# Kernel tuning notes

Measured on AMD Instinct MI355X. Metric: run time of the kernel, lower is better.

Reference implementation:

```python
import jax, jax.numpy as jnp
import numpy as np

B, D, F = 4096, 2048, 16384


def setup_inputs() -> dict:
    key = jax.random.key(0)
    ks = jax.random.split(key, 5)
    s_enc = 1.0 / np.sqrt(D)
    s_dec = 1.0 / np.sqrt(F)
    return {
        "x": jax.random.normal(ks[0], (B, D), dtype=jnp.float32),
        "W_enc": jax.random.normal(ks[1], (F, D), dtype=jnp.float32) * s_enc,
        "b_enc": jnp.zeros((F,), dtype=jnp.float32),
        "W_kest1": jax.random.normal(ks[2], (F, D), dtype=jnp.float32) * s_enc,
        "b_kest1": jnp.zeros((F,), dtype=jnp.float32),
        "W_kest2": jax.random.normal(ks[3], (1, F), dtype=jnp.float32) * s_dec,
        "b_kest2": jnp.zeros((1,), dtype=jnp.float32),
        "W_dec": jax.random.normal(ks[4], (D, F), dtype=jnp.float32) * s_dec,
        "b_dec": jnp.zeros((D,), dtype=jnp.float32),
        "k": 64,
    }


def topk_per_row(acts, k_est):
    # rank of each element when sorted descending (ties resolved stably;
    # after ReLU ties are zeros, so output is identical either way)
    order = jnp.argsort(-acts, axis=1)          # [B, F] descending order
    rank = jnp.argsort(order, axis=1)           # rank[i,j] = position of acts[i,j]
    mask = rank < k_est[:, None]                # per-row dynamic (float) k
    return acts * mask


def reference(x, W_enc, b_enc, W_kest1, b_kest1, W_kest2, b_kest2, W_dec, b_dec, k):
    xc = x - b_dec                                              # [B, D]
    acts = jax.nn.relu(xc @ W_enc.T + b_enc)                    # [B, F]
    h = jax.nn.relu(xc @ W_kest1.T + b_kest1)                   # [B, F]
    k_est = jax.nn.sigmoid(h @ W_kest2.T + b_kest2)[:, 0] * (2.0 * k)  # [B]
    enc = topk_per_row(acts, k_est)                             # [B, F] sparse codes
    x_hat = enc @ W_dec.T + b_dec                               # [B, D]
    return x_hat
```

## Files before the change

kernel.cpp:

```cpp
#include <hip/hip_runtime.h>
#include <hip/hip_bf16.h>
#include <cstdint>
#include <cstddef>

#define BATCH 4096
#define DIM   2048
#define FEAT  16384
#define MAXF  2048

typedef __attribute__((ext_vector_type(8))) short s8v;
typedef __attribute__((ext_vector_type(8))) _Float16 h8v;
typedef __attribute__((ext_vector_type(4))) float f4v;

__device__ __forceinline__ void split2(float v, unsigned short &h, unsigned short &l){
  _Float16 hf = (_Float16)v;
  _Float16 lf = (_Float16)((v - (float)hf) * 2048.0f);
  h = __builtin_bit_cast(unsigned short, hf);
  l = __builtin_bit_cast(unsigned short, lf);
}

__device__ __forceinline__ void gload16(const void* g, void* l){
  __builtin_amdgcn_global_load_lds(
      (const __attribute__((address_space(1))) void*)g,
      (__attribute__((address_space(3))) void*)l, 16, 0, 0);
}

__global__ __launch_bounds__(256)
void splitX(const float* __restrict__ x, const float* __restrict__ bdec,
            unsigned short* __restrict__ p0, unsigned short* __restrict__ p1)
{
  const size_t i = ((size_t)blockIdx.x * 256 + threadIdx.x) * 4;
  const int col = (int)(i & (DIM - 1));
  const float4 v = *(const float4*)(x + i);
  const float4 b = *(const float4*)(bdec + col);
  float e0 = v.x - b.x, e1 = v.y - b.y, e2 = v.z - b.z, e3 = v.w - b.w;
  ushort4 H, L;
  split2(e0, H.x, L.x); split2(e1, H.y, L.y);
  split2(e2, H.z, L.z); split2(e3, H.w, L.w);
  *(ushort4*)(p0 + i) = H; *(ushort4*)(p1 + i) = L;
}

__global__ __launch_bounds__(256)
void splitW(const float* __restrict__ w,
            unsigned short* __restrict__ p0, unsigned short* __restrict__ p1)
{
  const size_t i = ((size_t)blockIdx.x * 256 + threadIdx.x) * 4;
  const float4 v = *(const float4*)(w + i);
  ushort4 H, L;
  split2(v.x, H.x, L.x); split2(v.y, H.y, L.y);
  split2(v.z, H.z, L.z); split2(v.w, H.w, L.w);
  *(ushort4*)(p0 + i) = H; *(ushort4*)(p1 + i) = L;
}

__global__ __launch_bounds__(256)
void splitW1(const float* __restrict__ w, unsigned short* __restrict__ p0)
{
  const size_t i = ((size_t)blockIdx.x * 256 + threadIdx.x) * 4;
  const float4 v = *(const float4*)(w + i);
  ushort4 H;
  H.x = __builtin_bit_cast(unsigned short, (_Float16)v.x);
  H.y = __builtin_bit_cast(unsigned short, (_Float16)v.y);
  H.z = __builtin_bit_cast(unsigned short, (_Float16)v.z);
  H.w = __builtin_bit_cast(unsigned short, (_Float16)v.w);
  *(ushort4*)(p0 + i) = H;
}

__global__ __launch_bounds__(512, 3)
void gemmd(const unsigned short* __restrict__ Ah_, const unsigned short* __restrict__ B1h_,
           const unsigned short* __restrict__ B2h_,
           const float* __restrict__ benc, const float* __restrict__ bk1,
           const float* __restrict__ w2,
           float* __restrict__ acts, float* __restrict__ zpart)
{
  __shared__ unsigned short sAB[2][3][128][32];
  const int tid  = threadIdx.x;
  const int lane = tid & 63, wv = tid >> 6;

  const int bid = blockIdx.x;
  const int xcd = bid & 7;
  const int idx = bid >> 3;
  const int sq  = idx >> 6;
  const int s   = idx & 63;
  const int bx  = (xcd << 4) | ((sq & 1) << 3) | (s & 7);
  const int by  = ((sq >> 1) << 3) | (s >> 3);
  const int row0 = by << 7, col0 = bx << 7;

  const int role = wv >> 2;
  const int wloc = wv & 3;
  const int wr = (wloc & 1) << 6, wc = (wloc >> 1) << 6;

  f4v acc[4][4];
  #pragma unroll
  for (int i = 0; i < 4; ++i)
    #pragma unroll
    for (int j = 0; j < 4; ++j)
      acc[i][j] = (f4v){0.f, 0.f, 0.f, 0.f};

  const unsigned short* gsrc[3];
  unsigned ldsoff[3];
  #pragma unroll
  for (int j = 0; j < 3; ++j){
    const int q = wv * 3 + j;
    const int mat = q >> 3;
    const int chunk = q & 7;
    const int r  = (chunk << 4) + (lane >> 2);
    const int gl = (lane & 3) ^ ((r >> 1) & 3);
    const int rowg = ((mat == 0) ? row0 : col0) + r;
    const unsigned short* P = (mat == 0) ? Ah_ : ((mat == 1) ? B1h_ : B2h_);
    gsrc[j]  = P + (size_t)rowg * DIM + (gl << 3);
    ldsoff[j] = (unsigned)(mat * 8192 + chunk * 1024);
  }

  const int fr16 = lane & 15;
  const int kg   = lane >> 4;
  const int bmat = 1 + role;
  int ra[4], rb[4];
  #pragma unroll
  for (int f = 0; f < 4; ++f){ ra[f] = wr + (f << 4) + fr16; rb[f] = wc + (f << 4) + fr16; }

  #define LDFRAGD(bf, mat, r) \
    (*(const h8v*)((const char*)sAB + (bf) * 24576 + (mat) * 8192 + (r) * 64 + (((kg ^ (((r) >> 1) & 3)) << 4))))
  #define STAGED(bf, ko)                                                      \
    {                                                                         \
      _Pragma("unroll")                                                       \
      for (int j = 0; j < 3; ++j)                                             \
        gload16(gsrc[j] + (ko), (char*)sAB + (bf) * 24576 + ldsoff[j]);       \
    }

  int cur = 0;
  STAGED(0, 0);
  __syncthreads();

  for (int kt = 0; kt < DIM / 32; ++kt){
    if (kt < DIM / 32 - 1) STAGED(cur ^ 1, (kt + 1) << 5);

    h8v Ahf[4], Bhf[4];
    #pragma unroll
    for (int f = 0; f < 4; ++f) Ahf[f] = LDFRAGD(cur, 0, ra[f]);
    #pragma unroll
    for (int f = 0; f < 4; ++f) Bhf[f] = LDFRAGD(cur, bmat, rb[f]);
    #pragma unroll
    for (int fi = 0; fi < 4; ++fi)
      #pragma unroll
      for (int fj = 0; fj < 4; ++fj)
        acc[fi][fj] = __builtin_amdgcn_mfma_f32_16x16x32_f16(Bhf[fj], Ahf[fi], acc[fi][fj], 0, 0, 0);

    __syncthreads();
    cur ^= 1;
  }
  #undef LDFRAGD
  #undef STAGED

  const int mloc = lane & 15;
  const int nq   = (lane >> 4) << 2;
  if (role == 0){
    #pragma unroll
    for (int fi = 0; fi < 4; ++fi){
      const int grow = row0 + wr + (fi << 4) + mloc;
      #pragma unroll
      for (int fj = 0; fj < 4; ++fj){
        const int gcol = col0 + wc + (fj << 4) + nq;
        const float4 be = *(const float4*)(benc + gcol);
        f4v v;
        v[0] = fmaxf(acc[fi][fj][0] + be.x, 0.f);
        v[1] = fmaxf(acc[fi][fj][1] + be.y, 0.f);
        v[2] = fmaxf(acc[fi][fj][2] + be.z, 0.f);
        v[3] = fmaxf(acc[fi][fj][3] + be.w, 0.f);
        __builtin_nontemporal_store(v, (f4v*)(acts + (size_t)grow * FEAT + gcol));
      }
    }
  } else {
    #pragma unroll
    for (int fi = 0; fi < 4; ++fi){
      float ssum = 0.f;
      #pragma unroll
      for (int fj = 0; fj < 4; ++fj){
        const int gcol = col0 + wc + (fj << 4) + nq;
        const float4 be = *(const float4*)(bk1 + gcol);
        const float4 wk = *(const float4*)(w2 + gcol);
        float h0 = fmaxf(acc[fi][fj][0] + be.x, 0.f);
        float h1 = fmaxf(acc[fi][fj][1] + be.y, 0.f);
        float h2 = fmaxf(acc[fi][fj][2] + be.z, 0.f);
        float h3 = fmaxf(acc[fi][fj][3] + be.w, 0.f);
        ssum = fmaf(h0, wk.x, ssum);
        ssum = fmaf(h1, wk.y, ssum);
        ssum = fmaf(h2, wk.z, ssum);
        ssum = fmaf(h3, wk.w, ssum);
      }
      ssum += __shfl_xor(ssum, 16);
      ssum += __shfl_xor(ssum, 32);
      if (lane < 16){
        const int grow = row0 + wr + (fi << 4) + lane;
        zpart[(size_t)grow * 256 + (bx << 1) + (wc >> 6)] = ssum;
      }
    }
  }
}

__global__ __launch_bounds__(512, 4)
void gemmx(const unsigned short* __restrict__ Ah_, const unsigned short* __restrict__ Al_,
           const unsigned short* __restrict__ Bh_, const unsigned short* __restrict__ Bl_,
           const float* __restrict__ bias, const float* __restrict__ w2,
           const int* __restrict__ rowList, const int* __restrict__ nflagp,
           float* __restrict__ zexact)
{
  const int panel = blockIdx.x >> 7;
  const int bx    = blockIdx.x & 127;
  const int row0p = panel << 7;
  if (row0p >= *nflagp) return;
  const int col0 = bx << 7;

  __shared__ unsigned short sAB[2][2][128][64];
  const int tid  = threadIdx.x;
  const int lane = tid & 63, wv = tid >> 6;
  const int wr = (wv & 3) << 5, wc = (wv >> 2) << 6;

  f4v acc[2][4], acc2[2][4];
  #pragma unroll
  for (int i = 0; i < 2; ++i)
    #pragma unroll
    for (int j = 0; j < 4; ++j){
      acc[i][j]  = (f4v){0.f, 0.f, 0.f, 0.f};
      acc2[i][j] = (f4v){0.f, 0.f, 0.f, 0.f};
    }

  const unsigned short* gsrc[4];
  unsigned ldsoff[4];
  #pragma unroll
  for (int j = 0; j < 4; ++j){
    const int q = (wv << 2) + j;
    const int mat = q >> 4;
    const int chunk = q & 15;
    const int r  = (chunk << 3) + (lane >> 3);
    const int gl = (lane & 7) ^ (r & 7);
    const int co = (gl & 3) << 3;
    const unsigned short* hi = (mat == 0) ? Ah_ : Bh_;
    const unsigned short* lo = (mat == 0) ? Al_ : Bl_;
    const int rowg = (mat == 0) ? rowList[row0p + r] : (col0 + r);
    gsrc[j]  = ((gl < 4) ? hi : lo) + (size_t)rowg * DIM + co;
    ldsoff[j] = (unsigned)(mat * 16384 + chunk * 1024);
  }

  const int fr16 = lane & 15;
  const int kg   = lane >> 4;
  int ra[2], rb[4];
  #pragma unroll
  for (int f = 0; f < 2; ++f) ra[f] = wr + (f << 4) + fr16;
  #pragma unroll
  for (int f = 0; f < 4; ++f) rb[f] = wc + (f << 4) + fr16;

  #define LDFRAG(bf, mat, r, hb) \
    (*(const h8v*)((const char*)sAB + (bf) * 32768 + (mat) * 16384 + (r) * 128 + (((((hb) + kg) ^ ((r) & 7)) << 4))))
  #define STAGE(bf, ko)                                                       \
    {                                                                         \
      _Pragma("unroll")                                                       \
      for (int j = 0; j < 4; ++j)                                             \
        gload16(gsrc[j] + (ko), (char*)sAB + (bf) * 32768 + ldsoff[j]);       \
    }

  int cur = 0;
  STAGE(0, 0);
  __syncthreads();

  for (int kt = 0; kt < DIM / 32; ++kt){
    if (kt < DIM / 32 - 1) STAGE(cur ^ 1, (kt + 1) << 5);

    h8v Ahf[2], Bhf[4], Xl[4];
    #pragma unroll
    for (int f = 0; f < 2; ++f) Ahf[f] = LDFRAG(cur, 0, ra[f], 0);
    #pragma unroll
    for (int f = 0; f < 4; ++f) Bhf[f] = LDFRAG(cur, 1, rb[f], 0);
    #pragma unroll
    for (int fi = 0; fi < 2; ++fi)
      #pragma unroll
      for (int fj = 0; fj < 4; ++fj)
        acc[fi][fj] = __builtin_amdgcn_mfma_f32_16x16x32_f16(Bhf[fj], Ahf[fi], acc[fi][fj], 0, 0, 0);
    #pragma unroll
    for (int f = 0; f < 2; ++f) Xl[f] = LDFRAG(cur, 0, ra[f], 4);
    #pragma unroll
    for (int fi = 0; fi < 2; ++fi)
      #pragma unroll
      for (int fj = 0; fj < 4; ++fj)
        acc2[fi][fj] = __builtin_amdgcn_mfma_f32_16x16x32_f16(Bhf[fj], Xl[fi], acc2[fi][fj], 0, 0, 0);
    #pragma unroll
    for (int f = 0; f < 4; ++f) Xl[f] = LDFRAG(cur, 1, rb[f], 4);
    #pragma unroll
    for (int fi = 0; fi < 2; ++fi)
      #pragma unroll
      for (int fj = 0; fj < 4; ++fj)
        acc2[fi][fj] = __builtin_amdgcn_mfma_f32_16x16x32_f16(Xl[fj], Ahf[fi], acc2[fi][fj], 0, 0, 0);

    __syncthreads();
    cur ^= 1;
  }
  #undef LDFRAG
  #undef STAGE

  const float LSC = 1.0f / 2048.0f;
  const int nq = (lane >> 4) << 2;
  #pragma unroll
  for (int fi = 0; fi < 2; ++fi){
    float ssum = 0.f;
    #pragma unroll
    for (int fj = 0; fj < 4; ++fj){
      const int gcol = col0 + wc + (fj << 4) + nq;
      const float4 be = *(const float4*)(bias + gcol);
      const float4 wk = *(const float4*)(w2 + gcol);
      float h0 = fmaxf(acc[fi][fj][0] + LSC * acc2[fi][fj][0] + be.x, 0.f);
      float h1 = fmaxf(acc[fi][fj][1] + LSC * acc2[fi][fj][1] + be.y, 0.f);
      float h2 = fmaxf(acc[fi][fj][2] + LSC * acc2[fi][fj][2] + be.z, 0.f);
      float h3 = fmaxf(acc[fi][fj][3] + LSC * acc2[fi][fj][3] + be.w, 0.f);
      ssum = fmaf(h0, wk.x, ssum);
      ssum = fmaf(h1, wk.y, ssum);
      ssum = fmaf(h2, wk.z, ssum);
      ssum = fmaf(h3, wk.w, ssum);
    }
    ssum += __shfl_xor(ssum, 16);
    ssum += __shfl_xor(ssum, 32);
    if (lane < 16){
      const int pos = row0p + wr + (fi << 4) + lane;
      zexact[(size_t)pos * 256 + (bx << 1) + (wc >> 6)] = ssum;
    }
  }
}

__global__ __launch_bounds__(256)
void zinit(int* __restrict__ rowList, int* __restrict__ nflag)
{
  const int i = blockIdx.x * 256 + threadIdx.x;
  if (i < MAXF) rowList[i] = 0;
  if (i == 0) *nflag = 0;
}

__global__ __launch_bounds__(256)
void zreduce_flag(const float* __restrict__ zpart, const float* __restrict__ bk2,
                  const int* __restrict__ kp, int* __restrict__ mrow,
                  int* __restrict__ rowList, int* __restrict__ nflag)
{
  const int row  = blockIdx.x * 4 + (threadIdx.x >> 6);
  const int lane = threadIdx.x & 63;
  const float* zp = zpart + (size_t)row * 256;
  float s = zp[lane] + zp[lane + 64] + zp[lane + 128] + zp[lane + 192];
  s += __shfl_xor(s, 1);
  s += __shfl_xor(s, 2);
  s += __shfl_xor(s, 4);
  s += __shfl_xor(s, 8);
  s += __shfl_xor(s, 16);
  s += __shfl_xor(s, 32);
  if (lane == 0){
    float z = s + bk2[0];
    float kest = 2.f * (float)(*kp) * (1.f / (1.f + expf(-z)));
    int m = (int)ceilf(kest);
    m = min(max(m, 0), 128);
    mrow[row] = m;
    const float frac = kest - floorf(kest);
    const float dmin = fminf(frac, 1.f - frac);
    if (dmin < 0.1f){
      int p = atomicAdd(nflag, 1);
      if (p < MAXF) rowList[p] = row;
    }
  }
}

__global__ __launch_bounds__(256)
void zreduce2(const float* __restrict__ zexact, const int* __restrict__ rowList,
              const int* __restrict__ nflagp, const float* __restrict__ bk2,
              const int* __restrict__ kp, int* __restrict__ mrow)
{
  const int pos  = blockIdx.x * 4 + (threadIdx.x >> 6);
  const int lane = threadIdx.x & 63;
  const int nf = min(*nflagp, MAXF);
  if (pos >= nf) return;
  const float* zp = zexact + (size_t)pos * 256;
  float s = zp[lane] + zp[lane + 64] + zp[lane + 128] + zp[lane + 192];
  s += __shfl_xor(s, 1);
  s += __shfl_xor(s, 2);
  s += __shfl_xor(s, 4);
  s += __shfl_xor(s, 8);
  s += __shfl_xor(s, 16);
  s += __shfl_xor(s, 32);
  if (lane == 0){
    float z = s + bk2[0];
    float kest = 2.f * (float)(*kp) * (1.f / (1.f + expf(-z)));
    int m = (int)ceilf(kest);
    m = min(max(m, 0), 128);
    mrow[rowList[pos]] = m;
  }
}

__device__ __forceinline__ void radix_find(int* hist, int nbins, int need, int tid,
                                           int* out3, int* blksum)
{
  const int per  = nbins >> 8;
  const int base = tid * per;
  int bs = 0;
  for (int j = 0; j < per; ++j) bs += hist[base + j];
  blksum[tid] = bs;
  __syncthreads();
  if (tid == 0){
    int a2 = 0;
    for (int t = 255; t >= 0; --t){ int v = blksum[t]; blksum[t] = a2; a2 += v; }
  }
  __syncthreads();
  int ch = blksum[tid];
  for (int j = per - 1; j >= 0; --j){
    const int b = base + j;
    const int c = hist[b];
    if (ch < need && need <= ch + c){ out3[0] = b; out3[1] = need - ch; out3[2] = ch; }
    ch += c;
  }
  __syncthreads();
}

__global__ __launch_bounds__(256)
void select_band(const float* __restrict__ acts, const float* __restrict__ x,
                 const float* __restrict__ bdec, const float* __restrict__ Wenc,
                 const int* __restrict__ mrow, int* __restrict__ selIdx,
                 float* __restrict__ selVal, int* __restrict__ scount)
{
  __shared__ int hist[2048];
  __shared__ int blksum[256];
  __shared__ int out3[4];
  __shared__ unsigned listU[2048];
  __shared__ int listI[2048];
  __shared__ int lcnt, dcnt, acnt;
  __shared__ unsigned ambU[64];
  __shared__ int ambI[64];
  __shared__ double ambE[64];
  __shared__ double wred[4];

  const int row = blockIdx.x, tid = threadIdx.x;
  const int m = mrow[row];
  const float* rp = acts + (size_t)row * FEAT;
  const int base = row << 7;

  for (int i = tid; i < 2048; i += 256) hist[i] = 0;
  __syncthreads();
  for (int it = 0; it < 16; ++it){
    const int i4 = (it << 8) + tid;
    const uint4 u4 = *(const uint4*)(rp + ((size_t)i4 << 2));
    if (u4.x) atomicAdd(&hist[u4.x >> 21], 1);
    if (u4.y) atomicAdd(&hist[u4.y >> 21], 1);
    if (u4.z) atomicAdd(&hist[u4.z >> 21], 1);
    if (u4.w) atomicAdd(&hist[u4.w >> 21], 1);
  }
  __syncthreads();
  radix_find(hist, 2048, m, tid, out3, blksum);
  const int bin1 = out3[0];
  const int rem1 = out3[1];
  const int bin1m1 = (bin1 > 1) ? bin1 - 1 : 1;

  if (tid == 0){ lcnt = 0; dcnt = 0; acnt = 0; }
  __syncthreads();
  for (int it = 0; it < 16; ++it){
    const int i4 = (it << 8) + tid;
    const uint4 u4 = *(const uint4*)(rp + ((size_t)i4 << 2));
    const int ib = i4 << 2;
    if (u4.x && (int)(u4.x >> 21) >= bin1m1){ int p = atomicAdd(&lcnt, 1); if (p < 2048){ listU[p] = u4.x; listI[p] = ib;     } }
    if (u4.y && (int)(u4.y >> 21) >= bin1m1){ int p = atomicAdd(&lcnt, 1); if (p < 2048){ listU[p] = u4.y; listI[p] = ib + 1; } }
    if (u4.z && (int)(u4.z >> 21) >= bin1m1){ int p = atomicAdd(&lcnt, 1); if (p < 2048){ listU[p] = u4.z; listI[p] = ib + 2; } }
    if (u4.w && (int)(u4.w >> 21) >= bin1m1){ int p = atomicAdd(&lcnt, 1); if (p < 2048){ listU[p] = u4.w; listI[p] = ib + 3; } }
  }
  __syncthreads();
  const int L = min(lcnt, 2048);

  for (int i = tid; i < 2048; i += 256) hist[i] = 0;
  __syncthreads();
  for (int i = tid; i < L; i += 256){
    unsigned u = listU[i];
    if ((int)(u >> 21) == bin1) atomicAdd(&hist[(u >> 10) & 0x7FF], 1);
  }
  __syncthreads();
  radix_find(hist, 2048, rem1, tid, out3, blksum);
  const int bin2 = out3[0];
  const int rem2 = out3[1];

  const unsigned topbits = (((unsigned)bin1 << 11) | (unsigned)bin2);
  for (int i = tid; i < 1024; i += 256) hist[i] = 0;
  __syncthreads();
  for (int i = tid; i < L; i += 256){
    unsigned u = listU[i];
    if ((u >> 10) == topbits) atomicAdd(&hist[u & 0x3FF], 1);
  }
  __syncthreads();
  radix_find(hist, 1024, rem2, tid, out3, blksum);
  const int bin3 = out3[0];

  const unsigned tbits = ((unsigned)bin1 << 21) | ((unsigned)bin2 << 10) | (unsigned)bin3;
  const float vm = __uint_as_float(tbits);
  const float EPS2 = 0.01f;
  const float lo_cut = vm - EPS2, hi_cut = vm + EPS2;

  for (int i = tid; i < L; i += 256){
    const float f = __uint_as_float(listU[i]);
    if (f > hi_cut){
      int p = atomicAdd(&dcnt, 1);
      selIdx[base + p] = listI[i];
      selVal[base + p] = f;
    } else if (f >= lo_cut){
      int p = atomicAdd(&acnt, 1);
      if (p < 64){ ambU[p] = listU[i]; ambI[p] = listI[i]; }
    }
  }
  __syncthreads();
  const int D = dcnt;
  const int A = min(acnt, 64);
  int need = m - D;
  if (need < 0) need = 0;
  if (need > A) need = A;

  if (need > 0){
    float* xcs = (float*)hist;
    for (int j = tid; j < DIM; j += 256)
      xcs[j] = x[(size_t)row * DIM + j] - bdec[j];
    __syncthreads();
    const int lane = tid & 63, wv = tid >> 6;
    for (int c = 0; c < A; ++c){
      const float* wrow = Wenc + (size_t)ambI[c] * DIM;
      double sd = 0.0;
      for (int j = tid; j < DIM; j += 256)
        sd += (double)xcs[j] * (double)wrow[j];
      #pragma unroll
      for (int off = 32; off; off >>= 1) sd += __shfl_xor(sd, off);
      if (lane == 0) wred[wv] = sd;
      __syncthreads();
      if (tid == 0) ambE[c] = wred[0] + wred[1] + wred[2] + wred[3];
      __syncthreads();
    }
    if (tid == 0){
      for (int e = 0; e < need; ++e){
        int best = -1;
        for (int c = 0; c < A; ++c){
          if (ambI[c] < 0) continue;
          if (best < 0 || ambE[c] > ambE[best] ||
              (ambE[c] == ambE[best] && ambI[c] < ambI[best])) best = c;
        }
        selIdx[base + D + e] = ambI[best];
        selVal[base + D + e] = __uint_as_float(ambU[best]);
        ambI[best] = -1;
      }
    }
  }
  if (tid == 0) scount[row] = D + need;
}

__global__ __launch_bounds__(256)
void transpose_dec(const float* __restrict__ Wd, _Float16* __restrict__ WdT16)
{
  __shared__ float t[64][65];
  const int f0 = blockIdx.x << 6, d0 = blockIdx.y << 6;
  const int tx = threadIdx.x & 15, ty = threadIdx.x >> 4;
  #pragma unroll
  for (int r = 0; r < 4; ++r){
    const int d = ty + (r << 4);
    const float4 v = *(const float4*)(Wd + (size_t)(d0 + d) * FEAT + f0 + (tx << 2));
    t[d][(tx << 2) + 0] = v.x;
    t[d][(tx << 2) + 1] = v.y;
    t[d][(tx << 2) + 2] = v.z;
    t[d][(tx << 2) + 3] = v.w;
  }
  __syncthreads();
  #pragma unroll
  for (int r = 0; r < 4; ++r){
    const int f = ty + (r << 4);
    ushort4 o;
    o.x = __builtin_bit_cast(unsigned short, (_Float16)t[(tx << 2) + 0][f]);
    o.y = __builtin_bit_cast(unsigned short, (_Float16)t[(tx << 2) + 1][f]);
    o.z = __builtin_bit_cast(unsigned short, (_Float16)t[(tx << 2) + 2][f]);
    o.w = __builtin_bit_cast(unsigned short, (_Float16)t[(tx << 2) + 3][f]);
    *(ushort4*)(WdT16 + (size_t)(f0 + f) * DIM + d0 + (tx << 2)) = o;
  }
}

__global__ __launch_bounds__(256)
void decode_k(const _Float16* __restrict__ WdT16, const int* __restrict__ selIdx,
              const float* __restrict__ selVal, const int* __restrict__ scount,
              const float* __restrict__ bdec, float* __restrict__ out)
{
  __shared__ int   sI[128];
  __shared__ float sV[128];
  const int row = blockIdx.x, tid = threadIdx.x;
  const int m = scount[row];
  if (tid < m){
    sI[tid] = selIdx[(row << 7) + tid];
    sV[tid] = selVal[(row << 7) + tid];
  }
  __syncthreads();
  const int d = tid << 3;
  float a[8];
  {
    const float4 b0 = *(const float4*)(bdec + d);
    const float4 b1 = *(const float4*)(bdec + d + 4);
    a[0] = b0.x; a[1] = b0.y; a[2] = b0.z; a[3] = b0.w;
    a[4] = b1.x; a[5] = b1.y; a[6] = b1.z; a[7] = b1.w;
  }
  for (int i = 0; i < m; ++i){
    const float v = sV[i];
    const h8v w = *(const h8v*)(WdT16 + (size_t)sI[i] * DIM + d);
    #pragma unroll
    for (int j = 0; j < 8; ++j)
      a[j] = fmaf(v, (float)w[j], a[j]);
  }
  float4 o0 = {a[0], a[1], a[2], a[3]};
  float4 o1 = {a[4], a[5], a[6], a[7]};
  *(float4*)(out + (size_t)row * DIM + d)     = o0;
  *(float4*)(out + (size_t)row * DIM + d + 4) = o1;
}

extern "C" void kernel_launch(void* const* d_in, const int* in_sizes, int n_in,
                              void* d_out, int out_size, void* d_ws, size_t ws_size,
                              hipStream_t stream)
{
  const float* x    = (const float*)d_in[0];
  const float* Wenc = (const float*)d_in[1];
  const float* benc = (const float*)d_in[2];
  const float* Wk1  = (const float*)d_in[3];
  const float* bk1  = (const float*)d_in[4];
  const float* Wk2  = (const float*)d_in[5];
  const float* bk2  = (const float*)d_in[6];
  const float* Wdec = (const float*)d_in[7];
  const float* bdec = (const float*)d_in[8];
  const int*   kp   = (const int*)d_in[9];
  float* out = (float*)d_out;

  char* ws = (char*)d_ws;
  const size_t XS_BYTES   = (size_t)BATCH * DIM * 2;
  const size_t ACTS_BYTES = (size_t)BATCH * FEAT * 4;
  const size_t WP_BYTES   = (size_t)FEAT * DIM * 2;

  unsigned short* xs0 = (unsigned short*)ws;
  unsigned short* xs1 = (unsigned short*)(ws + XS_BYTES);
  char* p = ws + 2 * XS_BYTES;
  float* acts = (float*)p;
  _Float16* WdT16 = (_Float16*)p;
  p += ACTS_BYTES;
  unsigned short* wk0 = (unsigned short*)p;
  unsigned short* wk1 = (unsigned short*)(p + WP_BYTES);
  unsigned short* we0 = (unsigned short*)(p + 2 * WP_BYTES);
  p += 3 * WP_BYTES;
  float* zpart  = (float*)p;               p += 4194304;
  int*   mrow   = (int*)p;                 p += 16384;
  int*   selIdx = (int*)p;                 p += 2097152;
  float* selVal = (float*)p;               p += 2097152;
  int*   scount = (int*)p;                 p += 16384;
  int*   rowList= (int*)p;                 p += MAXF * 4;
  int*   nflag  = (int*)p;                 p += 128;
  float* zexact = (float*)p;               p += (size_t)MAXF * 256 * 4;

  (void)ws_size; (void)in_sizes; (void)n_in; (void)out_size;

  splitX<<<dim3(BATCH * DIM / 1024), dim3(256), 0, stream>>>(x, bdec, xs0, xs1);
  splitW<<<dim3(FEAT * DIM / 1024), dim3(256), 0, stream>>>(Wk1, wk0, wk1);
  splitW1<<<dim3(FEAT * DIM / 1024), dim3(256), 0, stream>>>(Wenc, we0);
  gemmd<<<dim3(4096), dim3(512), 0, stream>>>(xs0, we0, wk0, benc, bk1, Wk2,
                                              acts, zpart);
  zinit<<<dim3(MAXF / 256), dim3(256), 0, stream>>>(rowList, nflag);
  zreduce_flag<<<dim3(BATCH / 4), dim3(256), 0, stream>>>(zpart, bk2, kp, mrow,
                                                          rowList, nflag);
  gemmx<<<dim3(16 * 128), dim3(512), 0, stream>>>(xs0, xs1, wk0, wk1, bk1, Wk2,
                                                  rowList, nflag, zexact);
  zreduce2<<<dim3(MAXF / 4), dim3(256), 0, stream>>>(zexact, rowList, nflag,
                                                     bk2, kp, mrow);
  select_band<<<dim3(BATCH), dim3(256), 0, stream>>>(acts, x, bdec, Wenc, mrow,
                                                     selIdx, selVal, scount);
  transpose_dec<<<dim3(FEAT / 64, DIM / 64), dim3(256), 0, stream>>>(Wdec, WdT16);
  decode_k<<<dim3(BATCH), dim3(256), 0, stream>>>(WdT16, selIdx, selVal, scount, bdec, out);
}
```

Before: 1.167 ms.

## Store encoder activations as fp16 and share A fragments across both GEMMs

The dual GEMM now has each 256-thread block compute both the encoder and k-estimator products, reusing each loaded A fragment for two accumulator sets instead of splitting roles across eight waves. Encoder activations are written as fp16 instead of fp32, halving the acts write and the two reads in select_band. The radix selection is cut to a single 32-bin refinement over fp16 bit patterns. This raises register pressure (two 4x4 accumulator sets per thread) and makes the band threshold coarser, relying on the exact-recompute band to stay correct.

```diff
diff --git a/kernel.cpp b/kernel.cpp
--- a/kernel.cpp
+++ b/kernel.cpp
@@ -8,9 +8,9 @@
 #define FEAT  16384
 #define MAXF  2048
 
-typedef __attribute__((ext_vector_type(8))) short s8v;
 typedef __attribute__((ext_vector_type(8))) _Float16 h8v;
 typedef __attribute__((ext_vector_type(4))) float f4v;
+typedef __attribute__((ext_vector_type(4))) unsigned short us4v;
 
 __device__ __forceinline__ void split2(float v, unsigned short &h, unsigned short &l){
   _Float16 hf = (_Float16)v;
@@ -65,12 +65,12 @@
   *(ushort4*)(p0 + i) = H;
 }
 
-__global__ __launch_bounds__(512, 3)
+__global__ __launch_bounds__(256, 2)
 void gemmd(const unsigned short* __restrict__ Ah_, const unsigned short* __restrict__ B1h_,
            const unsigned short* __restrict__ B2h_,
            const float* __restrict__ benc, const float* __restrict__ bk1,
            const float* __restrict__ w2,
-           float* __restrict__ acts, float* __restrict__ zpart)
+           _Float16* __restrict__ acts16, float* __restrict__ zpart)
 {
   __shared__ unsigned short sAB[2][3][128][32];
   const int tid  = threadIdx.x;
@@ -85,22 +85,22 @@
   const int by  = ((sq >> 1) << 3) | (s >> 3);
   const int row0 = by << 7, col0 = bx << 7;
 
-  const int role = wv >> 2;
-  const int wloc = wv & 3;
-  const int wr = (wloc & 1) << 6, wc = (wloc >> 1) << 6;
-
-  f4v acc[4][4];
+  const int wr = (wv & 1) << 6, wc = (wv >> 1) << 6;
+
+  f4v acc1[4][4], acc2[4][4];
   #pragma unroll
   for (int i = 0; i < 4; ++i)
     #pragma unroll
-    for (int j = 0; j < 4; ++j)
-      acc[i][j] = (f4v){0.f, 0.f, 0.f, 0.f};
-
-  const unsigned short* gsrc[3];
-  unsigned ldsoff[3];
-  #pragma unroll
-  for (int j = 0; j < 3; ++j){
-    const int q = wv * 3 + j;
+    for (int j = 0; j < 4; ++j){
+      acc1[i][j] = (f4v){0.f, 0.f, 0.f, 0.f};
+      acc2[i][j] = (f4v){0.f, 0.f, 0.f, 0.f};
+    }
+
+  const unsigned short* gsrc[6];
+  unsigned ldsoff[6];
+  #pragma unroll
+  for (int j = 0; j < 6; ++j){
+    const int q = wv * 6 + j;
     const int mat = q >> 3;
     const int chunk = q & 7;
     const int r  = (chunk << 4) + (lane >> 2);
@@ -113,7 +113,6 @@
 
   const int fr16 = lane & 15;
   const int kg   = lane >> 4;
-  const int bmat = 1 + role;
   int ra[4], rb[4];
   #pragma unroll
   for (int f = 0; f < 4; ++f){ ra[f] = wr + (f << 4) + fr16; rb[f] = wc + (f << 4) + fr16; }
@@ -123,7 +122,7 @@
   #define STAGED(bf, ko)                                                      \
     {                                                                         \
       _Pragma("unroll")                                                       \
-      for (int j = 0; j < 3; ++j)                                             \
+      for (int j = 0; j < 6; ++j)                                             \
         gload16(gsrc[j] + (ko), (char*)sAB + (bf) * 24576 + ldsoff[j]);       \
     }
 
@@ -134,16 +133,23 @@
   for (int kt = 0; kt < DIM / 32; ++kt){
     if (kt < DIM / 32 - 1) STAGED(cur ^ 1, (kt + 1) << 5);
 
-    h8v Ahf[4], Bhf[4];
+    h8v Ahf[4], Bf[4];
     #pragma unroll
     for (int f = 0; f < 4; ++f) Ahf[f] = LDFRAGD(cur, 0, ra[f]);
     #pragma unroll
-    for (int f = 0; f < 4; ++f) Bhf[f] = LDFRAGD(cur, bmat, rb[f]);
+    for (int f = 0; f < 4; ++f) Bf[f] = LDFRAGD(cur, 1, rb[f]);
     #pragma unroll
     for (int fi = 0; fi < 4; ++fi)
       #pragma unroll
       for (int fj = 0; fj < 4; ++fj)
-        acc[fi][fj] = __builtin_amdgcn_mfma_f32_16x16x32_f16(Bhf[fj], Ahf[fi], acc[fi][fj], 0, 0, 0);
+        acc1[fi][fj] = __builtin_amdgcn_mfma_f32_16x16x32_f16(Bf[fj], Ahf[fi], acc1[fi][fj], 0, 0, 0);
+    #pragma unroll
+    for (int f = 0; f < 4; ++f) Bf[f] = LDFRAGD(cur, 2, rb[f]);
+    #pragma unroll
+    for (int fi = 0; fi < 4; ++fi)
+      #pragma unroll
+      for (int fj = 0; fj < 4; ++fj)
+        acc2[fi][fj] = __builtin_amdgcn_mfma_f32_16x16x32_f16(Bf[fj], Ahf[fi], acc2[fi][fj], 0, 0, 0);
 
     __syncthreads();
     cur ^= 1;
@@ -153,46 +159,43 @@
 
   const int mloc = lane & 15;
   const int nq   = (lane >> 4) << 2;
-  if (role == 0){
-    #pragma unroll
-    for (int fi = 0; fi < 4; ++fi){
-      const int grow = row0 + wr + (fi << 4) + mloc;
-      #pragma unroll
-      for (int fj = 0; fj < 4; ++fj){
-        const int gcol = col0 + wc + (fj << 4) + nq;
-        const float4 be = *(const float4*)(benc + gcol);
-        f4v v;
-        v[0] = fmaxf(acc[fi][fj][0] + be.x, 0.f);
-        v[1] = fmaxf(acc[fi][fj][1] + be.y, 0.f);
-        v[2] = fmaxf(acc[fi][fj][2] + be.z, 0.f);
-        v[3] = fmaxf(acc[fi][fj][3] + be.w, 0.f);
-        __builtin_nontemporal_store(v, (f4v*)(acts + (size_t)grow * FEAT + gcol));
-      }
-    }
-  } else {
-    #pragma unroll
-    for (int fi = 0; fi < 4; ++fi){
-      float ssum = 0.f;
-      #pragma unroll
-      for (int fj = 0; fj < 4; ++fj){
-        const int gcol = col0 + wc + (fj << 4) + nq;
-        const float4 be = *(const float4*)(bk1 + gcol);
-        const float4 wk = *(const float4*)(w2 + gcol);
-        float h0 = fmaxf(acc[fi][fj][0] + be.x, 0.f);
-        float h1 = fmaxf(acc[fi][fj][1] + be.y, 0.f);
-        float h2 = fmaxf(acc[fi][fj][2] + be.z, 0.f);
-        float h3 = fmaxf(acc[fi][fj][3] + be.w, 0.f);
-        ssum = fmaf(h0, wk.x, ssum);
-        ssum = fmaf(h1, wk.y, ssum);
-        ssum = fmaf(h2, wk.z, ssum);
-        ssum = fmaf(h3, wk.w, ssum);
-      }
-      ssum += __shfl_xor(ssum, 16);
-      ssum += __shfl_xor(ssum, 32);
-      if (lane < 16){
-        const int grow = row0 + wr + (fi << 4) + lane;
-        zpart[(size_t)grow * 256 + (bx << 1) + (wc >> 6)] = ssum;
-      }
+  #pragma unroll
+  for (int fi = 0; fi < 4; ++fi){
+    const int grow = row0 + wr + (fi << 4) + mloc;
+    #pragma unroll
+    for (int fj = 0; fj < 4; ++fj){
+      const int gcol = col0 + wc + (fj << 4) + nq;
+      const float4 be = *(const float4*)(benc + gcol);
+      us4v h;
+      h[0] = __builtin_bit_cast(unsigned short, (_Float16)fmaxf(acc1[fi][fj][0] + be.x, 0.f));
+      h[1] = __builtin_bit_cast(unsigned short, (_Float16)fmaxf(acc1[fi][fj][1] + be.y, 0.f));
+      h[2] = __builtin_bit_cast(unsigned short, (_Float16)fmaxf(acc1[fi][fj][2] + be.z, 0.f));
+      h[3] = __builtin_bit_cast(unsigned short, (_Float16)fmaxf(acc1[fi][fj][3] + be.w, 0.f));
+      __builtin_nontemporal_store(h, (us4v*)(acts16 + (size_t)grow * FEAT + gcol));
+    }
+  }
+  #pragma unroll
+  for (int fi = 0; fi < 4; ++fi){
+    float ssum = 0.f;
+    #pragma unroll
+    for (int fj = 0; fj < 4; ++fj){
+      const int gcol = col0 + wc + (fj << 4) + nq;
+      const float4 be = *(const float4*)(bk1 + gcol);
+      const float4 wk = *(const float4*)(w2 + gcol);
+      float h0 = fmaxf(acc2[fi][fj][0] + be.x, 0.f);
+      float h1 = fmaxf(acc2[fi][fj][1] + be.y, 0.f);
+      float h2 = fmaxf(acc2[fi][fj][2] + be.z, 0.f);
+      float h3 = fmaxf(acc2[fi][fj][3] + be.w, 0.f);
+      ssum = fmaf(h0, wk.x, ssum);
+      ssum = fmaf(h1, wk.y, ssum);
+      ssum = fmaf(h2, wk.z, ssum);
+      ssum = fmaf(h3, wk.w, ssum);
+    }
+    ssum += __shfl_xor(ssum, 16);
+    ssum += __shfl_xor(ssum, 32);
+    if (lane < 16){
+      const int grow = row0 + wr + (fi << 4) + lane;
+      zpart[(size_t)grow * 256 + (bx << 1) + (wc >> 6)] = ssum;
     }
   }
 }
@@ -413,7 +416,7 @@
 }
 
 __global__ __launch_bounds__(256)
-void select_band(const float* __restrict__ acts, const float* __restrict__ x,
+void select_band(const _Float16* __restrict__ acts16, const float* __restrict__ x,
                  const float* __restrict__ bdec, const float* __restrict__ Wenc,
                  const int* __restrict__ mrow, int* __restrict__ selIdx,
                  float* __restrict__ selVal, int* __restrict__ scount)
@@ -421,28 +424,32 @@
   __shared__ int hist[2048];
   __shared__ int blksum[256];
   __shared__ int out3[4];
-  __shared__ unsigned listU[2048];
+  __shared__ unsigned short listU[2048];
   __shared__ int listI[2048];
+  __shared__ int h32[32];
   __shared__ int lcnt, dcnt, acnt;
-  __shared__ unsigned ambU[64];
+  __shared__ unsigned short ambU[64];
   __shared__ int ambI[64];
   __shared__ double ambE[64];
   __shared__ double wred[4];
 
   const int row = blockIdx.x, tid = threadIdx.x;
   const int m = mrow[row];
-  const float* rp = acts + (size_t)row * FEAT;
+  const unsigned short* rp = (const unsigned short*)(acts16 + (size_t)row * FEAT);
   const int base = row << 7;
 
   for (int i = tid; i < 2048; i += 256) hist[i] = 0;
   __syncthreads();
-  for (int it = 0; it < 16; ++it){
-    const int i4 = (it << 8) + tid;
-    const uint4 u4 = *(const uint4*)(rp + ((size_t)i4 << 2));
-    if (u4.x) atomicAdd(&hist[u4.x >> 21], 1);
-    if (u4.y) atomicAdd(&hist[u4.y >> 21], 1);
-    if (u4.z) atomicAdd(&hist[u4.z >> 21], 1);
-    if (u4.w) atomicAdd(&hist[u4.w >> 21], 1);
+  for (int it = 0; it < 8; ++it){
+    const int i8 = (it << 8) + tid;
+    const uint4 u4 = *(const uint4*)(rp + i8 * 8);
+    #pragma unroll
+    for (int w = 0; w < 4; ++w){
+      const unsigned ww = (&u4.x)[w];
+      const unsigned a = ww & 0xFFFFu, b = ww >> 16;
+      if (a) atomicAdd(&hist[a >> 5], 1);
+      if (b) atomicAdd(&hist[b >> 5], 1);
+    }
   }
   __syncthreads();
   radix_find(hist, 2048, m, tid, out3, blksum);
@@ -451,48 +458,50 @@
   const int bin1m1 = (bin1 > 1) ? bin1 - 1 : 1;
 
   if (tid == 0){ lcnt = 0; dcnt = 0; acnt = 0; }
-  __syncthreads();
-  for (int it = 0; it < 16; ++it){
-    const int i4 = (it << 8) + tid;
-    const uint4 u4 = *(const uint4*)(rp + ((size_t)i4 << 2));
-    const int ib = i4 << 2;
-    if (u4.x && (int)(u4.x >> 21) >= bin1m1){ int p = atomicAdd(&lcnt, 1); if (p < 2048){ listU[p] = u4.x; listI[p] = ib;     } }
-    if (u4.y && (int)(u4.y >> 21) >= bin1m1){ int p = atomicAdd(&lcnt, 1); if (p < 2048){ listU[p] = u4.y; listI[p] = ib + 1; } }
-    if (u4.z && (int)(u4.z >> 21) >= bin1m1){ int p = atomicAdd(&lcnt, 1); if (p < 2048){ listU[p] = u4.z; listI[p] = ib + 2; } }
-    if (u4.w && (int)(u4.w >> 21) >= bin1m1){ int p = atomicAdd(&lcnt, 1); if (p < 2048){ listU[p] = u4.w; listI[p] = ib + 3; } }
+  if (tid < 32) h32[tid] = 0;
+  __syncthreads();
+  for (int it = 0; it < 8; ++it){
+    const int i8 = (it << 8) + tid;
+    const uint4 u4 = *(const uint4*)(rp + i8 * 8);
+    const int ib = i8 << 3;
+    #pragma unroll
+    for (int w = 0; w < 4; ++w){
+      const unsigned ww = (&u4.x)[w];
+      const unsigned a = ww & 0xFFFFu, b = ww >> 16;
+      if ((int)(a >> 5) >= bin1m1){
+        int p = atomicAdd(&lcnt, 1);
+        if (p < 2048){ listU[p] = (unsigned short)a; listI[p] = ib + 2 * w; }
+      }
+      if ((int)(b >> 5) >= bin1m1){
+        int p = atomicAdd(&lcnt, 1);
+        if (p < 2048){ listU[p] = (unsigned short)b; listI[p] = ib + 2 * w + 1; }
+      }
+    }
   }
   __syncthreads();
   const int L = min(lcnt, 2048);
 
-  for (int i = tid; i < 2048; i += 256) hist[i] = 0;
-  __syncthreads();
   for (int i = tid; i < L; i += 256){
-    unsigned u = listU[i];
-    if ((int)(u >> 21) == bin1) atomicAdd(&hist[(u >> 10) & 0x7FF], 1);
-  }
-  __syncthreads();
-  radix_find(hist, 2048, rem1, tid, out3, blksum);
-  const int bin2 = out3[0];
-  const int rem2 = out3[1];
-
-  const unsigned topbits = (((unsigned)bin1 << 11) | (unsigned)bin2);
-  for (int i = tid; i < 1024; i += 256) hist[i] = 0;
-  __syncthreads();
+    const unsigned u = listU[i];
+    if ((int)(u >> 5) == bin1) atomicAdd(&h32[u & 31], 1);
+  }
+  __syncthreads();
+  if (tid == 0){
+    int c = 0, b3 = 0;
+    for (int j = 31; j >= 0; --j){
+      c += h32[j];
+      if (c >= rem1){ b3 = j; break; }
+    }
+    out3[3] = b3;
+  }
+  __syncthreads();
+  const unsigned short vm16 = (unsigned short)(((unsigned)bin1 << 5) | (unsigned)out3[3]);
+  const float vmf = (float)__builtin_bit_cast(_Float16, vm16);
+  const float EPS2 = 0.01f;
+  const float lo_cut = vmf - EPS2, hi_cut = vmf + EPS2;
+
   for (int i = tid; i < L; i += 256){
-    unsigned u = listU[i];
-    if ((u >> 10) == topbits) atomicAdd(&hist[u & 0x3FF], 1);
-  }
-  __syncthreads();
-  radix_find(hist, 1024, rem2, tid, out3, blksum);
-  const int bin3 = out3[0];
-
-  const unsigned tbits = ((unsigned)bin1 << 21) | ((unsigned)bin2 << 10) | (unsigned)bin3;
-  const float vm = __uint_as_float(tbits);
-  const float EPS2 = 0.01f;
-  const float lo_cut = vm - EPS2, hi_cut = vm + EPS2;
-
-  for (int i = tid; i < L; i += 256){
-    const float f = __uint_as_float(listU[i]);
+    const float f = (float)__builtin_bit_cast(_Float16, listU[i]);
     if (f > hi_cut){
       int p = atomicAdd(&dcnt, 1);
       selIdx[base + p] = listI[i];
@@ -536,7 +545,7 @@
               (ambE[c] == ambE[best] && ambI[c] < ambI[best])) best = c;
         }
         selIdx[base + D + e] = ambI[best];
-        selVal[base + D + e] = __uint_as_float(ambU[best]);
+        selVal[base + D + e] = (float)__builtin_bit_cast(_Float16, ambU[best]);
         ambI[best] = -1;
       }
     }
@@ -631,8 +640,8 @@
   unsigned short* xs0 = (unsigned short*)ws;
   unsigned short* xs1 = (unsigned short*)(ws + XS_BYTES);
   char* p = ws + 2 * XS_BYTES;
-  float* acts = (float*)p;
-  _Float16* WdT16 = (_Float16*)p;
+  _Float16* acts16 = (_Float16*)p;
+  _Float16* WdT16  = (_Float16*)p;
   p += ACTS_BYTES;
   unsigned short* wk0 = (unsigned short*)p;
   unsigned short* wk1 = (unsigned short*)(p + WP_BYTES);
@@ -652,8 +661,8 @@
   splitX<<<dim3(BATCH * DIM / 1024), dim3(256), 0, stream>>>(x, bdec, xs0, xs1);
   splitW<<<dim3(FEAT * DIM / 1024), dim3(256), 0, stream>>>(Wk1, wk0, wk1);
   splitW1<<<dim3(FEAT * DIM / 1024), dim3(256), 0, stream>>>(Wenc, we0);
-  gemmd<<<dim3(4096), dim3(512), 0, stream>>>(xs0, we0, wk0, benc, bk1, Wk2,
-                                              acts, zpart);
+  gemmd<<<dim3(4096), dim3(256), 0, stream>>>(xs0, we0, wk0, benc, bk1, Wk2,
+                                              acts16, zpart);
   zinit<<<dim3(MAXF / 256), dim3(256), 0, stream>>>(rowList, nflag);
   zreduce_flag<<<dim3(BATCH / 4), dim3(256), 0, stream>>>(zpart, bk2, kp, mrow,
                                                           rowList, nflag);
@@ -661,7 +670,7 @@
                                                   rowList, nflag, zexact);
   zreduce2<<<dim3(MAXF / 4), dim3(256), 0, stream>>>(zexact, rowList, nflag,
                                                      bk2, kp, mrow);
-  select_band<<<dim3(BATCH), dim3(256), 0, stream>>>(acts, x, bdec, Wenc, mrow,
+  select_band<<<dim3(BATCH), dim3(256), 0, stream>>>(acts16, x, bdec, Wenc, mrow,
                                                      selIdx, selVal, scount);
   transpose_dec<<<dim3(FEAT / 64, DIM / 64), dim3(256), 0, stream>>>(Wdec, WdT16);
   decode_k<<<dim3(BATCH), dim3(256), 0, stream>>>(WdT16, selIdx, selVal, scount, bdec, out);
```

After: 1.127 ms. 3.5% less time.
